# Kernel tuning notes

Measured on AMD Instinct MI355X. Metric: run time of the kernel, lower is better.

## Reference

```python
import jax, jax.numpy as jnp
import numpy as np

NEG = -1000000.0  # mask fill value used by original sequence_mask

def setup_inputs() -> dict:
    key = jax.random.key(0)
    k1, k2, k3, k4 = jax.random.split(key, 4)
    B, S, D = 32, 2048, 64
    queries = jax.random.normal(k1, (B, S, D), dtype=jnp.float32)
    keys = jax.random.normal(k2, (B, S, D), dtype=jnp.float32)
    values = jax.random.normal(k3, (B, S, D), dtype=jnp.float32)
    valid_lens = jax.random.randint(k4, (B,), 1, S + 1, dtype=jnp.int64)
    return {"queries": queries, "keys": keys, "values": values, "valid_lens": valid_lens}

def reference(queries, keys, values, valid_lens):
    d = queries.shape[-1]
    # [B, Sq, Sk]
    scores = jnp.einsum('bqd,bkd->bqk', queries, keys) / jnp.sqrt(jnp.asarray(d, queries.dtype))
    # valid_lens is 1D: one length per batch row, broadcast over all query rows
    kv_idx = jnp.arange(scores.shape[-1])  # [Sk]
    mask = kv_idx[None, None, :] < valid_lens[:, None, None]  # [B,1,Sk] broadcast
    scores = jnp.where(mask, scores, jnp.asarray(NEG, scores.dtype))
    weights = jax.nn.softmax(scores, axis=-1)
    # dropout p=0.0 -> identity
    return jnp.einsum('bqk,bkd->bqd', weights, values)
```

## Files before the change

kernel.cpp:

```cpp
#include <hip/hip_runtime.h>
#include <hip/hip_bf16.h>

typedef __attribute__((ext_vector_type(8))) short bf16x8;
typedef __attribute__((ext_vector_type(4))) float f32x4;

#define BATCH 32
#define SEQ   2048
#define PSTR  20
#define KSTR  72
#define VSTR  36
#define LOG2E 1.44269504088896340736f
#define QSCALE (0.125f * LOG2E)
#define NEGL  (-1000000.0f * LOG2E)

__device__ __forceinline__ unsigned int pk2(float lo, float hi) {
    __hip_bfloat162 h2 = __float22bfloat162_rn(make_float2(lo, hi));
    return *reinterpret_cast<unsigned int*>(&h2);
}

__device__ __forceinline__ void dma16(const short* g, short* l) {
    __builtin_amdgcn_global_load_lds((const __attribute__((address_space(1))) void*)g,
                                     (__attribute__((address_space(3))) void*)l, 16, 0, 0);
}

__device__ __forceinline__ int pslot(int kp, int q) {
    const int kp2 = (kp & 0x1A) | ((kp & 1) << 2) | ((kp >> 2) & 1);
    return (kp2 << 4) + q;
}

__global__ void prep_vl(const int* __restrict__ VL, int* __restrict__ meta) {
    __shared__ int sv[BATCH];
    const int t = threadIdx.x;
    int odd = (t < 16) ? VL[2 * t + 1] : 0;
    const bool is64 = (__ballot(odd != 0) == 0ULL);
    if (t < BATCH) {
        int x = is64 ? VL[2 * t] : VL[t];
        x = x < 0 ? 0 : (x > SEQ ? SEQ : x);
        sv[t] = x;
    }
    __syncthreads();
    if (t < BATCH) {
        const int x = sv[t];
        int rank = 0;
        for (int j = 0; j < BATCH; ++j) {
            const int y = sv[j];
            rank += (y > x) || (y == x && j < t);
        }
        meta[rank] = x;
        meta[BATCH + rank] = t;
    }
}

__global__ __launch_bounds__(256) void prepkv(const float* __restrict__ Kp,
                                              const float* __restrict__ Vp,
                                              const int* __restrict__ VL,
                                              short* __restrict__ Kb,
                                              short* __restrict__ Vt,
                                              int* __restrict__ meta) {
    __shared__ unsigned int l[64 * VSTR];
    __shared__ int sv[BATCH];
    const int tid = threadIdx.x;
    if (blockIdx.x == BATCH * 32) {
        if (tid < 64) {
            int odd = (tid < 16) ? VL[2 * tid + 1] : 0;
            const bool is64 = (__ballot(odd != 0) == 0ULL);
            if (tid < BATCH) {
                int x = is64 ? VL[2 * tid] : VL[tid];
                x = x < 0 ? 0 : (x > SEQ ? SEQ : x);
                sv[tid] = x;
            }
            asm volatile("s_waitcnt lgkmcnt(0)" ::: "memory");
            if (tid < BATCH) {
                const int x = sv[tid];
                int rank = 0;
                for (int j = 0; j < BATCH; ++j) {
                    const int y = sv[j];
                    rank += (y > x) || (y == x && j < tid);
                }
                meta[rank] = x;
                meta[BATCH + rank] = tid;
            }
        }
        return;
    }
    const int b = blockIdx.x >> 5, kt = blockIdx.x & 31, kb = kt * 64;
    const float* Kv = Kp + ((size_t)b * SEQ + kb) * 64;
    const float* Vb = Vp + ((size_t)b * SEQ + kb) * 64;
    #pragma unroll
    for (int h = 0; h < 4; ++h) {
        const int c = tid + h * 256;
        const int row = c >> 4, col = (c & 15) * 4;
        f32x4 x = *(const f32x4*)(Kv + row * 64 + col);
        unsigned int* dst = (unsigned int*)(Kb + ((size_t)b * SEQ + kb + row) * 64 + col);
        dst[0] = pk2(x[0], x[1]); dst[1] = pk2(x[2], x[3]);
    }
    #pragma unroll
    for (int h = 0; h < 2; ++h) {
        const int u = tid + h * 256;
        const int d4 = (u & 3) + ((u >> 7) << 2);
        const int kp = (u >> 2) & 31;
        f32x4 a = *(const f32x4*)(Vb + (2 * kp) * 64 + d4 * 4);
        f32x4 c = *(const f32x4*)(Vb + (2 * kp + 1) * 64 + d4 * 4);
        #pragma unroll
        for (int j = 0; j < 4; ++j)
            l[(d4 * 4 + j) * VSTR + kp] = pk2(a[j], c[j]);
    }
    __syncthreads();
    const int d = tid >> 2, cg = tid & 3;
    unsigned int w[8];
    #pragma unroll
    for (int j = 0; j < 8; ++j) w[j] = l[d * VSTR + cg * 8 + j];
    unsigned int* dst = (unsigned int*)Vt + ((size_t)(b * 32 + kt) * 64 + d) * 32 + cg * 8;
    #pragma unroll
    for (int j = 0; j < 8; ++j) dst[j] = w[j];
}

__global__ __launch_bounds__(256, 4)
void attn_fwd(const float* __restrict__ Qp, const short* __restrict__ Kb,
              const short* __restrict__ Vt, const int* __restrict__ meta,
              float* __restrict__ Out) {
    constexpr int S = SEQ;
    __shared__ short bK2[2 * 64 * 64];
    __shared__ short bV2[2 * 64 * 64];
    __shared__ unsigned int lPt[4 * 512];

    const int tid  = threadIdx.x;
    const int wave = tid >> 6, lane = tid & 63;
    const int l15  = lane & 15, grp = lane >> 4;
    const int r7   = l15 & 7;

    const int g  = blockIdx.x >> 8;
    const int k8 = (blockIdx.x >> 5) & 7;
    const int qt = blockIdx.x & 31;
    const int slot = (g << 3) + ((g & 1) ? 7 - k8 : k8);

    const int vl = meta[slot], batch = meta[BATCH + slot];
    const int ntiles = (vl + 63) >> 6;

    const short* Kbb = Kb + (size_t)batch * S * 64;
    const short* Vtb = Vt + (size_t)batch * 32 * 4096;

    const int r8 = lane >> 3, s8 = lane & 7, csw = s8 ^ r8;
    const short* gK0 = Kbb + (wave * 16 + r8) * 64 + csw * 8;
    const short* gV0 = Vtb + (wave * 16 + r8) * 64 + csw * 8;
    short* lK0 = &bK2[wave * 16 * 64];
    short* lV0 = &bV2[wave * 16 * 64];

    bf16x8 qf[2];
    {
        const float* qb = Qp + ((size_t)batch * S + qt * 64 + wave * 16 + l15) * 64 + grp * 8;
        #pragma unroll
        for (int kf = 0; kf < 2; ++kf) {
            f32x4 a = *(const f32x4*)(qb + kf * 32);
            f32x4 c = *(const f32x4*)(qb + kf * 32 + 4);
            union { bf16x8 v; unsigned int u[4]; } qq;
            qq.u[0] = pk2(a[0] * QSCALE, a[1] * QSCALE);
            qq.u[1] = pk2(a[2] * QSCALE, a[3] * QSCALE);
            qq.u[2] = pk2(c[0] * QSCALE, c[1] * QSCALE);
            qq.u[3] = pk2(c[2] * QSCALE, c[3] * QSCALE);
            qf[kf] = qq.v;
        }
    }

    f32x4 o[4] = {{0.f,0.f,0.f,0.f},{0.f,0.f,0.f,0.f},{0.f,0.f,0.f,0.f},{0.f,0.f,0.f,0.f}};
    float lpart = 0.f;
    unsigned int* pw = &lPt[wave * 512];

    if (ntiles > 0) {
        dma16(gK0,          lK0);
        dma16(gK0 + 8 * 64, lK0 + 8 * 64);
        dma16(gV0,          lV0);
        dma16(gV0 + 8 * 64, lV0 + 8 * 64);
    }

    for (int kt = 0; kt < ntiles; ++kt) {
        __syncthreads();
        if (kt + 1 < ntiles) {
            const int nb = ((kt + 1) & 1) * 4096;
            const int ko = (kt + 1) * 4096;
            dma16(gK0 + ko,          lK0 + nb);
            dma16(gK0 + ko + 8 * 64, lK0 + nb + 8 * 64);
            dma16(gV0 + ko,          lV0 + nb);
            dma16(gV0 + ko + 8 * 64, lV0 + nb + 8 * 64);
        }
        const short* bK = &bK2[(kt & 1) * 4096];
        const short* bV = &bV2[(kt & 1) * 4096];

        f32x4 st[4] = {{0.f,0.f,0.f,0.f},{0.f,0.f,0.f,0.f},{0.f,0.f,0.f,0.f},{0.f,0.f,0.f,0.f}};
        #pragma unroll
        for (int kf = 0; kf < 2; ++kf) {
            #pragma unroll
            for (int ct = 0; ct < 4; ++ct) {
                bf16x8 kfr = *(const bf16x8*)&bK[((ct * 16 + l15) << 6) +
                                                 (((kf * 4 + grp) ^ r7) << 3)];
                st[ct] = __builtin_amdgcn_mfma_f32_16x16x32_bf16(kfr, qf[kf], st[ct], 0, 0, 0);
            }
        }

        if (kt == ntiles - 1 && (vl & 63) != 0) {
            const int kbase = kt * 64;
            #pragma unroll
            for (int ct = 0; ct < 4; ++ct)
                #pragma unroll
                for (int r = 0; r < 4; ++r) {
                    const bool valid = (kbase + ct * 16 + grp * 4 + r) < vl;
                    st[ct][r] = valid ? st[ct][r] : NEGL;
                }
        }

        #pragma unroll
        for (int ct = 0; ct < 4; ++ct) {
            #pragma unroll
            for (int r = 0; r < 4; ++r) {
                st[ct][r] = exp2f(st[ct][r]);
                lpart += st[ct][r];
            }
            #pragma unroll
            for (int a = 0; a < 2; ++a)
                pw[pslot(ct * 8 + grp * 2 + a, l15)] = pk2(st[ct][2 * a], st[ct][2 * a + 1]);
        }
        asm volatile("s_waitcnt lgkmcnt(0)" ::: "memory");

        #pragma unroll
        for (int kk = 0; kk < 2; ++kk) {
            union { bf16x8 v; unsigned int u[4]; } pf;
            #pragma unroll
            for (int jj = 0; jj < 4; ++jj)
                pf.u[jj] = pw[pslot(kk * 16 + grp * 4 + jj, l15)];
            #pragma unroll
            for (int dt = 0; dt < 4; ++dt) {
                bf16x8 vf = *(const bf16x8*)&bV[((dt * 16 + l15) << 6) +
                                                (((kk * 4 + grp) ^ r7) << 3)];
                o[dt] = __builtin_amdgcn_mfma_f32_16x16x32_bf16(vf, pf.v, o[dt], 0, 0, 0);
            }
        }
    }

    float lrun = lpart;
    lrun += __shfl_xor(lrun, 16);
    lrun += __shfl_xor(lrun, 32);

    const float inv = (lrun > 0.f) ? 1.0f / lrun : 0.f;
    const size_t orow = ((size_t)batch * S + qt * 64 + wave * 16 + l15) * 64;
    #pragma unroll
    for (int dt = 0; dt < 4; ++dt) {
        f32x4 w = o[dt];
        w[0] *= inv; w[1] *= inv; w[2] *= inv; w[3] *= inv;
        *(f32x4*)(Out + orow + dt * 16 + grp * 4) = w;
    }
}

__device__ __forceinline__ void load_tile_fb(const float* __restrict__ Kb,
                                             const float* __restrict__ Vb,
                                             int tid, f32x4 kv[4], f32x4 vv[4]) {
    #pragma unroll
    for (int h = 0; h < 4; ++h) {
        const int c = tid + h * 256;
        kv[h] = *(const f32x4*)(Kb + (c >> 4) * 64 + (c & 15) * 4);
    }
    #pragma unroll
    for (int h = 0; h < 2; ++h) {
        const int u  = tid + h * 256;
        const int d4 = (u & 3) + ((u >> 7) << 2);
        const int kp = (u >> 2) & 31;
        vv[2 * h]     = *(const f32x4*)(Vb + (2 * kp) * 64 + d4 * 4);
        vv[2 * h + 1] = *(const f32x4*)(Vb + (2 * kp + 1) * 64 + d4 * 4);
    }
}

__global__ __launch_bounds__(256, 4)
void attn_fb(const float* __restrict__ Qp, const float* __restrict__ Kp,
             const float* __restrict__ Vp, const int* __restrict__ meta,
             float* __restrict__ Out) {
    constexpr int S = SEQ;
    constexpr int qtiles = S >> 6;
    __shared__ short        lK [64 * KSTR];
    __shared__ unsigned int lVt[64 * VSTR];
    __shared__ unsigned int lPt[4 * 32 * PSTR];
    const int tid = threadIdx.x;
    const int wave = tid >> 6, lane = tid & 63;
    const int l15 = lane & 15, grp = lane >> 4;
    const int slot = blockIdx.x / qtiles, qt = blockIdx.x % qtiles;
    const int vl = meta[slot], batch = meta[BATCH + slot];
    const int ntiles = (vl + 63) >> 6;
    const float* Kb = Kp + (size_t)batch * S * 64;
    const float* Vb = Vp + (size_t)batch * S * 64;
    bf16x8 qf[2];
    {
        const float* qb = Qp + ((size_t)batch * S + qt * 64 + wave * 16 + l15) * 64 + grp * 8;
        #pragma unroll
        for (int kf = 0; kf < 2; ++kf) {
            f32x4 a = *(const f32x4*)(qb + kf * 32);
            f32x4 b = *(const f32x4*)(qb + kf * 32 + 4);
            union { bf16x8 v; unsigned int u[4]; } qq;
            qq.u[0] = pk2(a[0], a[1]); qq.u[1] = pk2(a[2], a[3]);
            qq.u[2] = pk2(b[0], b[1]); qq.u[3] = pk2(b[2], b[3]);
            qf[kf] = qq.v;
        }
    }
    f32x4 o[4] = {{0.f,0.f,0.f,0.f},{0.f,0.f,0.f,0.f},{0.f,0.f,0.f,0.f},{0.f,0.f,0.f,0.f}};
    float mrun = -INFINITY, lrun = 0.f;
    unsigned int* pw = &lPt[wave * 32 * PSTR];
    f32x4 kv[4], vv[4];
    if (ntiles > 0) load_tile_fb(Kb, Vb, tid, kv, vv);
    for (int kt = 0; kt < ntiles; ++kt) {
        const int kb = kt * 64;
        __syncthreads();
        #pragma unroll
        for (int h = 0; h < 4; ++h) {
            const int c = tid + h * 256;
            const int row = c >> 4, col = (c & 15) * 4;
            union { f32x4 f; float e[4]; } x; x.f = kv[h];
            unsigned int* dst = (unsigned int*)&lK[row * KSTR + col];
            dst[0] = pk2(x.e[0], x.e[1]); dst[1] = pk2(x.e[2], x.e[3]);
        }
        #pragma unroll
        for (int h = 0; h < 2; ++h) {
            const int u  = tid + h * 256;
            const int d4 = (u & 3) + ((u >> 7) << 2);
            const int kp = (u >> 2) & 31;
            union { f32x4 f; float e[4]; } a, b;
            a.f = vv[2 * h]; b.f = vv[2 * h + 1];
            #pragma unroll
            for (int j = 0; j < 4; ++j)
                lVt[(d4 * 4 + j) * VSTR + kp] = pk2(a.e[j], b.e[j]);
        }
        if (kt + 1 < ntiles) load_tile_fb(Kb + (size_t)(kb + 64) * 64, Vb + (size_t)(kb + 64) * 64, tid, kv, vv);
        __syncthreads();
        f32x4 st[4] = {{0.f,0.f,0.f,0.f},{0.f,0.f,0.f,0.f},{0.f,0.f,0.f,0.f},{0.f,0.f,0.f,0.f}};
        #pragma unroll
        for (int kf = 0; kf < 2; ++kf) {
            #pragma unroll
            for (int ct = 0; ct < 4; ++ct) {
                bf16x8 kfr = *(const bf16x8*)&lK[(ct * 16 + l15) * KSTR + kf * 32 + grp * 8];
                st[ct] = __builtin_amdgcn_mfma_f32_16x16x32_bf16(kfr, qf[kf], st[ct], 0, 0, 0);
            }
        }
        #pragma unroll
        for (int ct = 0; ct < 4; ++ct)
            #pragma unroll
            for (int r = 0; r < 4; ++r) {
                const bool valid = (kb + ct * 16 + grp * 4 + r) < vl;
                st[ct][r] = valid ? st[ct][r] * (0.125f * LOG2E) : NEGL;
            }
        float t0 = fmaxf(fmaxf(st[0][0], st[0][1]), fmaxf(st[0][2], st[0][3]));
        float t1 = fmaxf(fmaxf(st[1][0], st[1][1]), fmaxf(st[1][2], st[1][3]));
        float t2 = fmaxf(fmaxf(st[2][0], st[2][1]), fmaxf(st[2][2], st[2][3]));
        float t3 = fmaxf(fmaxf(st[3][0], st[3][1]), fmaxf(st[3][2], st[3][3]));
        float tm = fmaxf(fmaxf(t0, t1), fmaxf(t2, t3));
        tm = fmaxf(tm, __shfl_xor(tm, 16));
        tm = fmaxf(tm, __shfl_xor(tm, 32));
        const float mnew  = fmaxf(mrun, tm);
        const float alpha = exp2f(mrun - mnew);
        mrun = mnew;
        lrun *= alpha;
        #pragma unroll
        for (int dt = 0; dt < 4; ++dt)
            #pragma unroll
            for (int r = 0; r < 4; ++r) o[dt][r] *= alpha;
        float rs = 0.f;
        #pragma unroll
        for (int ct = 0; ct < 4; ++ct) {
            #pragma unroll
            for (int r = 0; r < 4; ++r) {
                st[ct][r] = exp2f(st[ct][r] - mrun);
                rs += st[ct][r];
            }
            #pragma unroll
            for (int a = 0; a < 2; ++a)
                pw[(ct * 8 + grp * 2 + a) * PSTR + l15] = pk2(st[ct][2 * a], st[ct][2 * a + 1]);
        }
        rs += __shfl_xor(rs, 16);
        rs += __shfl_xor(rs, 32);
        lrun += rs;
        asm volatile("s_waitcnt lgkmcnt(0)" ::: "memory");
        #pragma unroll
        for (int kk = 0; kk < 2; ++kk) {
            union { bf16x8 v; unsigned int u[4]; } pf;
            #pragma unroll
            for (int jj = 0; jj < 4; ++jj)
                pf.u[jj] = pw[(kk * 16 + grp * 4 + jj) * PSTR + l15];
            #pragma unroll
            for (int dt = 0; dt < 4; ++dt) {
                bf16x8 vf = *(const bf16x8*)&lVt[(dt * 16 + l15) * VSTR + kk * 16 + grp * 4];
                o[dt] = __builtin_amdgcn_mfma_f32_16x16x32_bf16(vf, pf.v, o[dt], 0, 0, 0);
            }
        }
    }
    const float inv = (lrun > 0.f) ? 1.0f / lrun : 0.f;
    const size_t orow = ((size_t)batch * S + qt * 64 + wave * 16 + l15) * 64;
    #pragma unroll
    for (int dt = 0; dt < 4; ++dt) {
        f32x4 w = o[dt];
        w[0] *= inv; w[1] *= inv; w[2] *= inv; w[3] *= inv;
        *(f32x4*)(Out + orow + dt * 16 + grp * 4) = w;
    }
}

extern "C" void kernel_launch(void* const* d_in, const int* in_sizes, int n_in,
                              void* d_out, int out_size, void* d_ws, size_t ws_size,
                              hipStream_t stream) {
    const float* Q  = (const float*)d_in[0];
    const float* K  = (const float*)d_in[1];
    const float* V  = (const float*)d_in[2];
    const int*   VL = (const int*)d_in[3];
    int* meta = (int*)d_ws;
    const size_t need = 512 + 2 * (size_t)BATCH * SEQ * 64 * sizeof(short);
    dim3 block(256);
    if (ws_size >= need) {
        short* Kb = (short*)((char*)d_ws + 512);
        short* Vt = Kb + (size_t)BATCH * SEQ * 64;
        prepkv<<<dim3(BATCH * 32 + 1), block, 0, stream>>>(K, V, VL, Kb, Vt, meta);
        attn_fwd<<<dim3(BATCH * 32), block, 0, stream>>>(Q, Kb, Vt, meta, (float*)d_out);
    } else {
        prep_vl<<<1, 64, 0, stream>>>(VL, meta);
        attn_fb<<<dim3(BATCH * (SEQ >> 6)), block, 0, stream>>>(Q, K, V, meta, (float*)d_out);
    }
}
```

Before: 131.9 us.

## Switch attention to 32x32x16 MFMA with key-split waves and permlane P transpose

Replaces the 16x16x32 MFMA tiling with 32x32x16 MFMAs where each wave handles 32 queries by 32 keys of a tile (query half × key half split), moving P from accumulator layout to operand layout via v_permlane32_swap instead of an LDS round-trip. The per-wave partial outputs and row sums of the two key halves are merged through shared memory at the end. Waves whose key half lies entirely beyond valid_len skip the work. This removes the P LDS buffer and its waits and uses larger MFMAs, at the cost of a final cross-wave reduction and more accumulator registers.

```diff
diff --git a/kernel.cpp b/kernel.cpp
--- a/kernel.cpp
+++ b/kernel.cpp
@@ -3,6 +3,7 @@
 
 typedef __attribute__((ext_vector_type(8))) short bf16x8;
 typedef __attribute__((ext_vector_type(4))) float f32x4;
+typedef __attribute__((ext_vector_type(16))) float f32x16;
 
 #define BATCH 32
 #define SEQ   2048
@@ -23,9 +24,8 @@
                                      (__attribute__((address_space(3))) void*)l, 16, 0, 0);
 }
 
-__device__ __forceinline__ int pslot(int kp, int q) {
-    const int kp2 = (kp & 0x1A) | ((kp & 1) << 2) | ((kp >> 2) & 1);
-    return (kp2 << 4) + q;
+__device__ __forceinline__ void plswap(unsigned int& a, unsigned int& b) {
+    asm volatile("v_permlane32_swap_b32 %0, %1" : "+v"(a), "+v"(b));
 }
 
 __global__ void prep_vl(const int* __restrict__ VL, int* __restrict__ meta) {
@@ -122,12 +122,11 @@
     constexpr int S = SEQ;
     __shared__ short bK2[2 * 64 * 64];
     __shared__ short bV2[2 * 64 * 64];
-    __shared__ unsigned int lPt[4 * 512];
 
     const int tid  = threadIdx.x;
     const int wave = tid >> 6, lane = tid & 63;
-    const int l15  = lane & 15, grp = lane >> 4;
-    const int r7   = l15 & 7;
+    const int r31 = lane & 31, hi = lane >> 5;
+    const int qh = wave >> 1, kh = wave & 1;
 
     const int g  = blockIdx.x >> 8;
     const int k8 = (blockIdx.x >> 5) & 7;
@@ -146,13 +145,13 @@
     short* lK0 = &bK2[wave * 16 * 64];
     short* lV0 = &bV2[wave * 16 * 64];
 
-    bf16x8 qf[2];
+    bf16x8 qf[4];
     {
-        const float* qb = Qp + ((size_t)batch * S + qt * 64 + wave * 16 + l15) * 64 + grp * 8;
-        #pragma unroll
-        for (int kf = 0; kf < 2; ++kf) {
-            f32x4 a = *(const f32x4*)(qb + kf * 32);
-            f32x4 c = *(const f32x4*)(qb + kf * 32 + 4);
+        const float* qb = Qp + ((size_t)batch * S + qt * 64 + qh * 32 + r31) * 64 + hi * 8;
+        #pragma unroll
+        for (int kf = 0; kf < 4; ++kf) {
+            f32x4 a = *(const f32x4*)(qb + kf * 16);
+            f32x4 c = *(const f32x4*)(qb + kf * 16 + 4);
             union { bf16x8 v; unsigned int u[4]; } qq;
             qq.u[0] = pk2(a[0] * QSCALE, a[1] * QSCALE);
             qq.u[1] = pk2(a[2] * QSCALE, a[3] * QSCALE);
@@ -162,9 +161,12 @@
         }
     }
 
-    f32x4 o[4] = {{0.f,0.f,0.f,0.f},{0.f,0.f,0.f,0.f},{0.f,0.f,0.f,0.f},{0.f,0.f,0.f,0.f}};
+    f32x16 o[2];
+    #pragma unroll
+    for (int dt = 0; dt < 2; ++dt)
+        #pragma unroll
+        for (int r = 0; r < 16; ++r) o[dt][r] = 0.f;
     float lpart = 0.f;
-    unsigned int* pw = &lPt[wave * 512];
 
     if (ntiles > 0) {
         dma16(gK0,          lK0);
@@ -172,6 +174,9 @@
         dma16(gV0,          lV0);
         dma16(gV0 + 8 * 64, lV0 + 8 * 64);
     }
+
+    const int krow = kh * 32 + r31;
+    const int l7 = lane & 7;
 
     for (int kt = 0; kt < ntiles; ++kt) {
         __syncthreads();
@@ -183,70 +188,96 @@
             dma16(gV0 + ko,          lV0 + nb);
             dma16(gV0 + ko + 8 * 64, lV0 + nb + 8 * 64);
         }
-        const short* bK = &bK2[(kt & 1) * 4096];
-        const short* bV = &bV2[(kt & 1) * 4096];
-
-        f32x4 st[4] = {{0.f,0.f,0.f,0.f},{0.f,0.f,0.f,0.f},{0.f,0.f,0.f,0.f},{0.f,0.f,0.f,0.f}};
-        #pragma unroll
-        for (int kf = 0; kf < 2; ++kf) {
-            #pragma unroll
-            for (int ct = 0; ct < 4; ++ct) {
-                bf16x8 kfr = *(const bf16x8*)&bK[((ct * 16 + l15) << 6) +
-                                                 (((kf * 4 + grp) ^ r7) << 3)];
-                st[ct] = __builtin_amdgcn_mfma_f32_16x16x32_bf16(kfr, qf[kf], st[ct], 0, 0, 0);
-            }
-        }
-
-        if (kt == ntiles - 1 && (vl & 63) != 0) {
-            const int kbase = kt * 64;
-            #pragma unroll
-            for (int ct = 0; ct < 4; ++ct)
+        const char* bK = (const char*)&bK2[(kt & 1) * 4096];
+        const char* bV = (const char*)&bV2[(kt & 1) * 4096];
+
+        if (kt * 64 + kh * 32 < vl) {
+            f32x16 st;
+            #pragma unroll
+            for (int r = 0; r < 16; ++r) st[r] = 0.f;
+            #pragma unroll
+            for (int kf = 0; kf < 4; ++kf) {
+                bf16x8 kfr = *(const bf16x8*)(bK + krow * 128 +
+                                              (((kf * 2 + hi) ^ l7) << 4));
+                st = __builtin_amdgcn_mfma_f32_32x32x16_bf16(kfr, qf[kf], st, 0, 0, 0);
+            }
+
+            if (kt == ntiles - 1 && (vl & 63) != 0) {
+                const int kb = kt * 64 + kh * 32 + 4 * hi;
                 #pragma unroll
-                for (int r = 0; r < 4; ++r) {
-                    const bool valid = (kbase + ct * 16 + grp * 4 + r) < vl;
-                    st[ct][r] = valid ? st[ct][r] : NEGL;
+                for (int r = 0; r < 16; ++r) {
+                    const int key = kb + (r & 3) + 8 * (r >> 2);
+                    st[r] = (key < vl) ? st[r] : NEGL;
                 }
-        }
-
-        #pragma unroll
-        for (int ct = 0; ct < 4; ++ct) {
-            #pragma unroll
-            for (int r = 0; r < 4; ++r) {
-                st[ct][r] = exp2f(st[ct][r]);
-                lpart += st[ct][r];
-            }
-            #pragma unroll
-            for (int a = 0; a < 2; ++a)
-                pw[pslot(ct * 8 + grp * 2 + a, l15)] = pk2(st[ct][2 * a], st[ct][2 * a + 1]);
-        }
-        asm volatile("s_waitcnt lgkmcnt(0)" ::: "memory");
-
-        #pragma unroll
-        for (int kk = 0; kk < 2; ++kk) {
-            union { bf16x8 v; unsigned int u[4]; } pf;
-            #pragma unroll
-            for (int jj = 0; jj < 4; ++jj)
-                pf.u[jj] = pw[pslot(kk * 16 + grp * 4 + jj, l15)];
-            #pragma unroll
-            for (int dt = 0; dt < 4; ++dt) {
-                bf16x8 vf = *(const bf16x8*)&bV[((dt * 16 + l15) << 6) +
-                                                (((kk * 4 + grp) ^ r7) << 3)];
-                o[dt] = __builtin_amdgcn_mfma_f32_16x16x32_bf16(vf, pf.v, o[dt], 0, 0, 0);
-            }
-        }
-    }
-
-    float lrun = lpart;
-    lrun += __shfl_xor(lrun, 16);
-    lrun += __shfl_xor(lrun, 32);
-
-    const float inv = (lrun > 0.f) ? 1.0f / lrun : 0.f;
-    const size_t orow = ((size_t)batch * S + qt * 64 + wave * 16 + l15) * 64;
-    #pragma unroll
-    for (int dt = 0; dt < 4; ++dt) {
-        f32x4 w = o[dt];
-        w[0] *= inv; w[1] *= inv; w[2] *= inv; w[3] *= inv;
-        *(f32x4*)(Out + orow + dt * 16 + grp * 4) = w;
+            }
+
+            #pragma unroll
+            for (int r = 0; r < 16; ++r) st[r] = exp2f(st[r]);
+            {
+                const float a0 = (st[0] + st[1]) + (st[2] + st[3]);
+                const float a1 = (st[4] + st[5]) + (st[6] + st[7]);
+                const float a2 = (st[8] + st[9]) + (st[10] + st[11]);
+                const float a3 = (st[12] + st[13]) + (st[14] + st[15]);
+                lpart += (a0 + a1) + (a2 + a3);
+            }
+
+            union { bf16x8 v; unsigned int u[4]; } pf0, pf1;
+            {
+                unsigned int x0 = pk2(st[0], st[1]),   y0 = pk2(st[4], st[5]);
+                unsigned int x1 = pk2(st[2], st[3]),   y1 = pk2(st[6], st[7]);
+                plswap(x0, y0); plswap(x1, y1);
+                pf0.u[0] = x0; pf0.u[1] = x1; pf0.u[2] = y0; pf0.u[3] = y1;
+                unsigned int x2 = pk2(st[8], st[9]),   y2 = pk2(st[12], st[13]);
+                unsigned int x3 = pk2(st[10], st[11]), y3 = pk2(st[14], st[15]);
+                plswap(x2, y2); plswap(x3, y3);
+                pf1.u[0] = x2; pf1.u[1] = x3; pf1.u[2] = y2; pf1.u[3] = y3;
+            }
+
+            #pragma unroll
+            for (int dt = 0; dt < 2; ++dt) {
+                const int vrow = dt * 32 + r31;
+                bf16x8 vf0 = *(const bf16x8*)(bV + vrow * 128 +
+                                              (((kh * 4 + hi) ^ l7) << 4));
+                o[dt] = __builtin_amdgcn_mfma_f32_32x32x16_bf16(vf0, pf0.v, o[dt], 0, 0, 0);
+                bf16x8 vf1 = *(const bf16x8*)(bV + vrow * 128 +
+                                              (((kh * 4 + 2 + hi) ^ l7) << 4));
+                o[dt] = __builtin_amdgcn_mfma_f32_32x32x16_bf16(vf1, pf1.v, o[dt], 0, 0, 0);
+            }
+        }
+    }
+
+    float lw = lpart + __shfl_xor(lpart, 32);
+
+    __syncthreads();
+    float* mrg = (float*)bK2;
+    float* lm  = (float*)bV2;
+    if (kh == 1) {
+        #pragma unroll
+        for (int dt = 0; dt < 2; ++dt)
+            #pragma unroll
+            for (int r = 0; r < 16; ++r)
+                mrg[qh * 2048 + (dt * 16 + r) * 64 + lane] = o[dt][r];
+        lm[qh * 64 + lane] = lw;
+    }
+    __syncthreads();
+    if (kh == 0) {
+        #pragma unroll
+        for (int dt = 0; dt < 2; ++dt)
+            #pragma unroll
+            for (int r = 0; r < 16; ++r)
+                o[dt][r] += mrg[qh * 2048 + (dt * 16 + r) * 64 + lane];
+        lw += lm[qh * 64 + lane];
+        const float inv = (lw > 0.f) ? 1.0f / lw : 0.f;
+        const size_t orow = ((size_t)batch * S + qt * 64 + qh * 32 + r31) * 64;
+        #pragma unroll
+        for (int dt = 0; dt < 2; ++dt)
+            #pragma unroll
+            for (int g4 = 0; g4 < 4; ++g4) {
+                f32x4 w;
+                #pragma unroll
+                for (int j = 0; j < 4; ++j) w[j] = o[dt][g4 * 4 + j] * inv;
+                *(f32x4*)(Out + orow + dt * 32 + g4 * 8 + hi * 4) = w;
+            }
     }
 }
 
```

Result: faster. 127.9 us (-3.0%).
